# Kernel tuning notes

Hardware: AMD Instinct MI355X
Metric: run time of the kernel (lower is better)

Reference implementation:

```python
import jax, jax.numpy as jnp
import numpy as np

DIM = 512
HID = 1024        # dim * expansion_factor
QK = 128          # query_key_dim
G = 256           # group_size
EPS = 1e-5


def setup_inputs() -> dict:
    key = jax.random.key(0)
    ks = jax.random.split(key, 6)
    x = jax.random.normal(ks[0], (4, 4096, DIM), jnp.float32)
    ln_w = jnp.ones((DIM,), jnp.float32)
    ln_b = jnp.zeros((DIM,), jnp.float32)
    Wh = 0.02 * jax.random.normal(ks[1], (DIM, 2 * HID), jnp.float32)
    bh = jnp.zeros((2 * HID,), jnp.float32)
    Wqk = 0.02 * jax.random.normal(ks[2], (DIM, QK), jnp.float32)
    bqk = jnp.zeros((QK,), jnp.float32)
    gamma = 0.02 * jax.random.normal(ks[3], (4, QK), jnp.float32)  # nn.init.normal_(gamma, std=0.02)
    beta = jnp.zeros((4, QK), jnp.float32)
    Wo = 0.02 * jax.random.normal(ks[4], (HID, DIM), jnp.float32)
    bo = jnp.zeros((DIM,), jnp.float32)
    return {"x": x, "ln_w": ln_w, "ln_b": ln_b, "Wh": Wh, "bh": bh,
            "Wqk": Wqk, "bqk": bqk, "gamma": gamma, "beta": beta,
            "Wo": Wo, "bo": bo}


def reference(x, ln_w, ln_b, Wh, bh, Wqk, bqk, gamma, beta, Wo, bo):
    b, n, _ = x.shape
    g = n // G  # number of groups (n chosen as multiple of G -> no padding)

    # LayerNorm (torch uses biased variance)
    mu = jnp.mean(x, axis=-1, keepdims=True)
    var = jnp.mean((x - mu) ** 2, axis=-1, keepdims=True)
    normed = (x - mu) * jax.lax.rsqrt(var + EPS) * ln_w + ln_b

    # to_hidden: Linear -> SiLU, split into v / gate
    h = jax.nn.silu(normed @ Wh + bh)            # [b, n, 2*HID]
    v, gate = jnp.split(h, 2, axis=-1)           # each [b, n, HID]

    # to_qk: Linear -> SiLU, then 4-head offset/scale
    qk = jax.nn.silu(normed @ Wqk + bqk)         # [b, n, QK]
    qkh = qk[..., None, :] * gamma + beta        # [b, n, 4, QK]
    quad_q, lin_q, quad_k, lin_k = (qkh[..., i, :] for i in range(4))

    # group: b (g n) d -> b g n d
    grp = lambda t: t.reshape(b, g, G, t.shape[-1])
    qq, qk_, lq, lk, vv = map(grp, (quad_q, quad_k, lin_q, lin_k, v))

    # quadratic (group-local) attention with ReLU^2 scores, causal within group
    sim = jnp.einsum('bgid,bgjd->bgij', qq, qk_) / G
    attn = jnp.square(jnp.maximum(sim, 0.0))
    causal_mask = jnp.triu(jnp.ones((G, G), dtype=bool), 1)
    attn = jnp.where(causal_mask, 0.0, attn)
    quad_out = jnp.einsum('bgij,bgje->bgie', attn, vv)   # [b, g, G, HID]

    # linear attention across groups: per-group kv, exclusive cumsum over group dim
    lin_kv = jnp.einsum('bgnd,bgne->bgde', lk, vv) / G   # [b, g, QK, HID]
    lin_kv = jnp.cumsum(lin_kv, axis=1)
    lin_kv = jnp.pad(lin_kv, ((0, 0), (1, 0), (0, 0), (0, 0)))[:, :-1]
    lin_out = jnp.einsum('bgde,bgnd->bgne', lin_kv, lq)  # [b, g, G, HID]

    out = gate * (quad_out.reshape(b, n, HID) + lin_out.reshape(b, n, HID))
    return out @ Wo + bo + x
```

## Files before the change

### kernel.cpp

```cpp
#include <hip/hip_runtime.h>
#include <hip/hip_bf16.h>
#include <math.h>


#define BATCH 4
#define SEQ   4096
#define TROWS 16384
#define DIMD  512
#define HIDD  1024
#define QKD   128
#define GRP   256
#define NGRP  16
#define BGRP  64
#define EPIW  132
#define EPB   130

typedef unsigned short bfraw;
typedef __attribute__((ext_vector_type(8))) short bf16x8;
typedef __attribute__((ext_vector_type(8))) unsigned short u16x8;
typedef __attribute__((ext_vector_type(4))) unsigned int u32x4;
typedef __attribute__((ext_vector_type(4))) float f32x4;

__device__ __forceinline__ float bf2f(bfraw u) {
    union { float f; unsigned int i; } c;
    c.i = ((unsigned int)u) << 16;
    return c.f;
}
__device__ __forceinline__ bfraw f2bf(float f) {
    unsigned int x = __float_as_uint(f);
    unsigned int r = (x + 0x7fffu + ((x >> 16) & 1u)) >> 16;
    return (bfraw)r;
}
__device__ __forceinline__ unsigned int pkbf(float lo, float hi) {
    __hip_bfloat162 h2 = __float22bfloat162_rn(make_float2(lo, hi));
    union { __hip_bfloat162 h; unsigned int u; } c; c.h = h2;
    return c.u;
}
__device__ __forceinline__ void store16bf(bfraw* dst, const float* src) {
    u32x4 a, b;
    #pragma unroll
    for (int k = 0; k < 4; ++k) a[k] = pkbf(src[2 * k], src[2 * k + 1]);
    #pragma unroll
    for (int k = 0; k < 4; ++k) b[k] = pkbf(src[8 + 2 * k], src[8 + 2 * k + 1]);
    *(u32x4*)dst = a;
    *(u32x4*)(dst + 8) = b;
}
__device__ __forceinline__ float silu_f(float z) {
    return z / (1.f + __expf(-z));
}
__device__ __forceinline__ void gload_lds16(const void* g, void* l) {
    __builtin_amdgcn_global_load_lds(
        (const __attribute__((address_space(1))) unsigned int*)g,
        (__attribute__((address_space(3))) unsigned int*)l, 16, 0, 0);
}

__device__ __forceinline__ void mfma_step(const bfraw* As, const bfraw* Bs,
                                          f32x4 acc[4][4], int wm, int wn,
                                          int q, int mi) {
    bf16x8 af[4], bfg[4];
    #pragma unroll
    for (int i = 0; i < 4; ++i)
        af[i] = *(const bf16x8*)&As[(size_t)(wm * 64 + i * 16 + mi) * 32 + q * 8];
    #pragma unroll
    for (int j = 0; j < 4; ++j)
        bfg[j] = *(const bf16x8*)&Bs[(size_t)(wn * 64 + j * 16 + mi) * 32 + q * 8];
    #pragma unroll
    for (int i = 0; i < 4; ++i)
        #pragma unroll
        for (int j = 0; j < 4; ++j)
            acc[i][j] = __builtin_amdgcn_mfma_f32_16x16x32_bf16(af[i], bfg[j], acc[i][j], 0, 0, 0);
}

#define SMEMP_DECL                                              \
    __shared__ __align__(16) char smem_[33280];                 \
    bfraw* A0buf = (bfraw*)smem_;                               \
    bfraw* B0buf = (bfraw*)(smem_ + 8192);                      \
    bfraw* A1buf = (bfraw*)(smem_ + 16384);                     \
    bfraw* B1buf = (bfraw*)(smem_ + 24576);

#define PIPE_DSTS                                               \
    bfraw* a0d  = A0buf + wid * 512;                            \
    bfraw* a0d2 = A0buf + 2048 + wid * 512;                     \
    bfraw* b0d  = B0buf + wid * 512;                            \
    bfraw* b0d2 = B0buf + 2048 + wid * 512;                     \
    bfraw* a1d  = A1buf + wid * 512;                            \
    bfraw* a1d2 = A1buf + 2048 + wid * 512;                     \
    bfraw* b1d  = B1buf + wid * 512;                            \
    bfraw* b1d2 = B1buf + 2048 + wid * 512;

#define KLOOP_PRE(Abase, Astr, Bbase, Bstr)                                    \
    const bfraw* pa0 = (Abase) + (size_t)(t >> 2) * (Astr) + (t & 3) * 8;      \
    const bfraw* pa1 = pa0 + (size_t)64 * (Astr);                              \
    const bfraw* pb0 = (Bbase) + (size_t)(t >> 2) * (Bstr) + (t & 3) * 8;      \
    const bfraw* pb1 = pb0 + (size_t)64 * (Bstr);

#define STAGE0                                                                 \
    do { gload_lds16(pa0, a0d); gload_lds16(pa1, a0d2);                        \
         gload_lds16(pb0, b0d); gload_lds16(pb1, b0d2);                        \
         pa0 += 32; pa1 += 32; pb0 += 32; pb1 += 32; } while (0)
#define STAGE1                                                                 \
    do { gload_lds16(pa0, a1d); gload_lds16(pa1, a1d2);                        \
         gload_lds16(pb0, b1d); gload_lds16(pb1, b1d2);                        \
         pa0 += 32; pa1 += 32; pb0 += 32; pb1 += 32; } while (0)

#define PIPE_LOOP(NIT, Abase, Astr, Bbase, Bstr)                               \
    {                                                                          \
        KLOOP_PRE(Abase, Astr, Bbase, Bstr)                                    \
        STAGE0;                                                                \
        for (int it = 0; it < (NIT); it += 2) {                                \
            __syncthreads();                                                   \
            if (it + 1 < (NIT)) STAGE1;                                        \
            mfma_step(A0buf, B0buf, acc, wm, wn, q, mi);                       \
            __syncthreads();                                                   \
            if (it + 2 < (NIT)) STAGE0;                                        \
            if (it + 1 < (NIT))                                                \
                mfma_step(A1buf, B1buf, acc, wm, wn, q, mi);                   \
        }                                                                      \
        __syncthreads();                                                       \
    }

__device__ __forceinline__ int epi_row(int p, int lr) {
    return (lr < 16) ? (p * 16 + lr) : (64 + p * 16 + (lr - 16));
}

__global__ __launch_bounds__(256) void prep_kernel(const float* __restrict__ x,
                                                   const float* __restrict__ lnw,
                                                   const float* __restrict__ lnb,
                                                   const float* __restrict__ Wh,
                                                   const float* __restrict__ Wo,
                                                   const float* __restrict__ Wqk,
                                                   bfraw* __restrict__ normb,
                                                   bfraw* __restrict__ WhT,
                                                   bfraw* __restrict__ WoT,
                                                   bfraw* __restrict__ WqkT) {
    __shared__ float tile[32][33];
    int bid = blockIdx.x;
    int t = threadIdx.x;
    if (bid < 4096) {
        int row  = bid * 4 + (t >> 6);
        int lane = t & 63;
        const float* xr = x + (size_t)row * DIMD;
        float4 v0 = ((const float4*)xr)[lane];
        float4 v1 = ((const float4*)xr)[lane + 64];
        float s  = v0.x + v0.y + v0.z + v0.w + v1.x + v1.y + v1.z + v1.w;
        float ss = v0.x*v0.x + v0.y*v0.y + v0.z*v0.z + v0.w*v0.w
                 + v1.x*v1.x + v1.y*v1.y + v1.z*v1.z + v1.w*v1.w;
        #pragma unroll
        for (int off = 32; off; off >>= 1) {
            s  += __shfl_xor(s, off);
            ss += __shfl_xor(ss, off);
        }
        float mu  = s * (1.f / DIMD);
        float var = ss * (1.f / DIMD) - mu * mu;
        float inv = rsqrtf(var + 1e-5f);
        float4 w0 = ((const float4*)lnw)[lane],  w1 = ((const float4*)lnw)[lane + 64];
        float4 b0 = ((const float4*)lnb)[lane],  b1 = ((const float4*)lnb)[lane + 64];
        unsigned int o0 = pkbf((v0.x - mu) * inv * w0.x + b0.x,
                               (v0.y - mu) * inv * w0.y + b0.y);
        unsigned int o1 = pkbf((v0.z - mu) * inv * w0.z + b0.z,
                               (v0.w - mu) * inv * w0.w + b0.w);
        unsigned int o2 = pkbf((v1.x - mu) * inv * w1.x + b1.x,
                               (v1.y - mu) * inv * w1.y + b1.y);
        unsigned int o3 = pkbf((v1.z - mu) * inv * w1.z + b1.z,
                               (v1.w - mu) * inv * w1.w + b1.w);
        unsigned int* brow = (unsigned int*)(normb + (size_t)row * DIMD);
        ((uint2*)brow)[lane]      = make_uint2(o0, o1);
        ((uint2*)brow)[lane + 64] = make_uint2(o2, o3);
        return;
    }
    bid -= 4096;
    const float* in; bfraw* outp; int R, C, nx;
    if (bid < 1024)      { in = Wh;  outp = WhT;  R = DIMD; C = 2 * HIDD; nx = 64; }
    else if (bid < 1536) { bid -= 1024; in = Wo;  outp = WoT;  R = HIDD; C = DIMD; nx = 16; }
    else                 { bid -= 1536; in = Wqk; outp = WqkT; R = DIMD; C = QKD;  nx = 4; }
    int c0 = (bid % nx) * 32, r0 = (bid / nx) * 32;
    int tr = t >> 3, tc4 = (t & 7) * 4;
    float4 v = *(const float4*)&in[(size_t)(r0 + tr) * C + c0 + tc4];
    tile[tr][tc4 + 0] = v.x; tile[tr][tc4 + 1] = v.y;
    tile[tr][tc4 + 2] = v.z; tile[tr][tc4 + 3] = v.w;
    __syncthreads();
    ushort4 s;
    s.x = f2bf(tile[tc4 + 0][tr]);
    s.y = f2bf(tile[tc4 + 1][tr]);
    s.z = f2bf(tile[tc4 + 2][tr]);
    s.w = f2bf(tile[tc4 + 3][tr]);
    *(ushort4*)&outp[(size_t)(c0 + tr) * R + r0 + tc4] = s;
}

__global__ __launch_bounds__(512, 2) void gemm_h256(
    const bfraw* __restrict__ A,
    const bfraw* __restrict__ WhT,
    const bfraw* __restrict__ WqkT,
    const float* __restrict__ bh,
    const float* __restrict__ bqk,
    const float* __restrict__ gamma,
    const float* __restrict__ beta,
    bfraw* __restrict__ vT,
    bfraw* __restrict__ gate,
    bfraw* __restrict__ qq,
    bfraw* __restrict__ lq,
    bfraw* __restrict__ kk,
    bfraw* __restrict__ lkT) {
    __shared__ __align__(16) char smem_[131072];
    const int t = threadIdx.x;
    const int lane = t & 63, wid = t >> 6;
    const int wm = wid >> 2, wn = wid & 3;
    const int q = lane >> 4, mi = lane & 15;
    int nid = (blockIdx.x & 7) * 72 + (blockIdx.x >> 3);
    const int ct = nid % 9, by = nid / 9;
    const int r0 = by * 256, c0 = ct * 256;

    const int lslot = (lane & 7) ^ (lane >> 3);
    const int rbase = wid * 16 + (lane >> 3) * 2 + (lslot >> 2);
    const int kel   = (lslot & 3) * 8;
    const bfraw* As0 = A + (size_t)(r0 + rbase) * DIMD + kel;
    const bfraw* As1 = As0 + (size_t)128 * DIMD;
    const bfraw* Bs0; const bfraw* Bs1;
    if (ct < 8) {
        Bs0 = WhT + (size_t)(c0 + rbase) * DIMD + kel;
        Bs1 = Bs0 + (size_t)128 * DIMD;
    } else {
        Bs0 = WqkT + (size_t)rbase * DIMD + kel;
        Bs1 = Bs0;
    }
    const int swz = ((((mi & 1) << 2) | q) ^ ((mi >> 1) & 7)) << 4;
    const int a_off = (wm * 64 + (mi >> 1)) * 128 + swz;
    const int b_off = (wn * 32 + (mi >> 1)) * 128 + swz;
    const int ldst = wid * 1024;

#define GH_STAGE(KT, SLOT)                                                    \
    do {                                                                      \
        char* sb_ = smem_ + (SLOT) * 32768;                                   \
        gload_lds16(As0 + (KT) * 32, sb_ + ldst);                             \
        gload_lds16(As1 + (KT) * 32, sb_ + 8192 + ldst);                      \
        gload_lds16(Bs0 + (KT) * 32, sb_ + 16384 + ldst);                     \
        gload_lds16(Bs1 + (KT) * 32, sb_ + 24576 + ldst);                     \
    } while (0)

    f32x4 acc[8][4] = {};
    GH_STAGE(0, 0);
    GH_STAGE(1, 1);
    GH_STAGE(2, 2);
    asm volatile("s_waitcnt vmcnt(8)" ::: "memory");
    __builtin_amdgcn_s_barrier();

    #pragma unroll
    for (int j = 0; j < 16; ++j) {
        if (j + 3 < 16) GH_STAGE(j + 3, (j + 3) & 3);
        const char* cb = smem_ + (j & 3) * 32768;
        bf16x8 af[8], bfr[4];
        #pragma unroll
        for (int mf = 0; mf < 8; ++mf)
            af[mf] = *(const bf16x8*)(cb + a_off + mf * 1024);
        #pragma unroll
        for (int nf = 0; nf < 4; ++nf)
            bfr[nf] = *(const bf16x8*)(cb + 16384 + b_off + nf * 1024);
        __builtin_amdgcn_s_setprio(1);
        #pragma unroll
        for (int mf = 0; mf < 8; ++mf)
            #pragma unroll
            for (int nf = 0; nf < 4; ++nf)
                acc[mf][nf] = __builtin_amdgcn_mfma_f32_16x16x32_bf16(
                    af[mf], bfr[nf], acc[mf][nf], 0, 0, 0);
        __builtin_amdgcn_s_setprio(0);
        if (j + 3 < 16)      asm volatile("s_waitcnt vmcnt(8)" ::: "memory");
        else if (j + 2 < 16) asm volatile("s_waitcnt vmcnt(4)" ::: "memory");
        else if (j + 1 < 16) asm volatile("s_waitcnt vmcnt(0)" ::: "memory");
        __builtin_amdgcn_s_barrier();
    }
#undef GH_STAGE

    float* epi = (float*)smem_;
    if (ct == 8) {
        float* gbl = (float*)(smem_ + 33792);
        gbl[t] = gamma[t];
        gbl[t + 512] = beta[t];
        float bq4[4];
        #pragma unroll
        for (int nf = 0; nf < 4; ++nf)
            bq4[nf] = (wn < 2) ? bqk[wn * 64 + nf * 16 + mi] : 0.f;
        #pragma unroll
        for (int p = 0; p < 4; ++p) {
            if (wm == (p >> 1) && wn < 2) {
                #pragma unroll
                for (int m2 = 0; m2 < 4; ++m2) {
                    int mf = ((p & 1) << 2) + m2;
                    #pragma unroll
                    for (int nf = 0; nf < 4; ++nf)
                        #pragma unroll
                        for (int rg = 0; rg < 4; ++rg)
                            epi[(m2 * 16 + q * 4 + rg) * 132 + wn * 64 + nf * 16 + mi] =
                                silu_f(acc[mf][nf][rg] + bq4[nf]);
                }
            }
            __syncthreads();
            {
                int lr = t >> 3, cs = (t & 7) * 16;
                float z[16];
                #pragma unroll
                for (int k = 0; k < 16; ++k) z[k] = epi[lr * 132 + cs + k];
                size_t growr = (size_t)(r0 + p * 64 + lr) * QKD + cs;
                #pragma unroll
                for (int hd = 0; hd < 3; ++hd) {
                    bfraw* arr = (hd == 0) ? qq : (hd == 1) ? lq : kk;
                    float tmp[16];
                    #pragma unroll
                    for (int k = 0; k < 16; ++k)
                        tmp[k] = z[k] * gbl[hd * 128 + cs + k] + gbl[512 + hd * 128 + cs + k];
                    store16bf(arr + growr, tmp);
                }
            }
            {
                int c = t >> 2, jh = (t & 3) * 16;
                float g3 = gbl[384 + c], e3 = gbl[896 + c];
                float tmp[16];
                #pragma unroll
                for (int k = 0; k < 16; ++k)
                    tmp[k] = epi[(jh + k) * 132 + c] * g3 + e3;
                store16bf(lkT + ((size_t)by * QKD + c) * GRP + p * 64 + jh, tmp);
            }
            __syncthreads();
        }
        return;
    }
    float bias4[4];
    #pragma unroll
    for (int nf = 0; nf < 4; ++nf)
        bias4[nf] = bh[c0 + wn * 64 + nf * 16 + mi];
    if (ct < 4) {
        #pragma unroll
        for (int p = 0; p < 4; ++p) {
            if (wm == (p >> 1)) {
                #pragma unroll
                for (int m2 = 0; m2 < 4; ++m2) {
                    int mf = ((p & 1) << 2) + m2;
                    #pragma unroll
                    for (int nf = 0; nf < 4; ++nf)
                        #pragma unroll
                        for (int rg = 0; rg < 4; ++rg)
                            epi[(m2 * 16 + q * 4 + rg) * 257 + wn * 64 + nf * 16 + mi] =
                                silu_f(acc[mf][nf][rg] + bias4[nf]);
                }
            }
            __syncthreads();
            int e2 = t >> 1, js = (t & 1) * 32;
            bfraw* dst = vT + ((size_t)by * HIDD + c0 + e2) * GRP + p * 64 + js;
            #pragma unroll
            for (int h2 = 0; h2 < 2; ++h2) {
                float tmp[16];
                #pragma unroll
                for (int k = 0; k < 16; ++k)
                    tmp[k] = epi[(js + h2 * 16 + k) * 257 + e2];
                store16bf(dst + h2 * 16, tmp);
            }
            __syncthreads();
        }
    } else {
        #pragma unroll
        for (int p = 0; p < 4; ++p) {
            if (wm == (p >> 1)) {
                #pragma unroll
                for (int m2 = 0; m2 < 4; ++m2) {
                    int mf = ((p & 1) << 2) + m2;
                    #pragma unroll
                    for (int nf = 0; nf < 4; ++nf)
                        #pragma unroll
                        for (int rg = 0; rg < 4; ++rg)
                            epi[(m2 * 16 + q * 4 + rg) * 260 + wn * 64 + nf * 16 + mi] =
                                silu_f(acc[mf][nf][rg] + bias4[nf]);
                }
            }
            __syncthreads();
            int lr = t >> 3, cs = (t & 7) * 32;
            const float* src = epi + lr * 260 + cs;
            bfraw* dst = gate + (size_t)(r0 + p * 64 + lr) * HIDD + (c0 - HIDD) + cs;
            #pragma unroll
            for (int h2 = 0; h2 < 2; ++h2) {
                float tmp[16];
                #pragma unroll
                for (int k = 0; k < 16; ++k) tmp[k] = src[h2 * 16 + k];
                store16bf(dst + h2 * 16, tmp);
            }
            __syncthreads();
        }
    }
}

__global__ __launch_bounds__(256) void simkv_kernel(const bfraw* __restrict__ qq,
                                                    const bfraw* __restrict__ kk,
                                                    bfraw* __restrict__ attn,
                                                    const bfraw* __restrict__ vT,
                                                    const bfraw* __restrict__ lkT,
                                                    bfraw* __restrict__ kvT_raw) {
    SMEMP_DECL
    float* epi = (float*)smem_;
    int t = threadIdx.x;
    int lane = t & 63, wid = t >> 6;
    int wm = wid >> 1, wn = wid & 1;
    int q = lane >> 4, mi = lane & 15;
    int bid = blockIdx.x;
    f32x4 acc[4][4] = {};
    PIPE_DSTS
    if (bid < 512) {
        int bg = bid >> 3;
        int row0 = (bid & 7) * 128;
        PIPE_LOOP(8, vT + (size_t)bg * HIDD * GRP + (size_t)row0 * GRP, GRP,
                  lkT + (size_t)bg * QKD * GRP, GRP)
        bfraw* outg = kvT_raw + (size_t)bg * HIDD * QKD;
        #pragma unroll
        for (int p = 0; p < 4; ++p) {
            #pragma unroll
            for (int j = 0; j < 4; ++j)
                #pragma unroll
                for (int rg = 0; rg < 4; ++rg)
                    epi[(wm * 16 + q * 4 + rg) * EPIW + wn * 64 + j * 16 + mi] = acc[p][j][rg];
            __syncthreads();
            int lr = t >> 3, c0t = (t & 7) * 16;
            int gr = row0 + epi_row(p, lr);
            store16bf(outg + (size_t)gr * QKD + c0t, &epi[lr * EPIW + c0t]);
            __syncthreads();
        }
        return;
    }
    int i = bid - 512;
    int bg = i & 63;
    int tid = i >> 6;
    int ry = (tid == 0) ? 0 : 1;
    int rx = (tid == 2) ? 1 : 0;
    int row0 = ry * 128, col0 = rx * 128;
    PIPE_LOOP(4, qq + (size_t)(bg * GRP + row0) * QKD, QKD,
              kk + (size_t)(bg * GRP + col0) * QKD, QKD)
    bfraw* ag = attn + (size_t)bg * GRP * GRP;
    #pragma unroll
    for (int p = 0; p < 4; ++p) {
        #pragma unroll
        for (int j = 0; j < 4; ++j) {
            int colg = col0 + wn * 64 + j * 16 + mi;
            #pragma unroll
            for (int rg = 0; rg < 4; ++rg) {
                int rowg = row0 + wm * 64 + p * 16 + q * 4 + rg;
                float s = acc[p][j][rg] * (1.f / GRP);
                s = fmaxf(s, 0.f);
                s = s * s;
                epi[(wm * 16 + q * 4 + rg) * EPIW + wn * 64 + j * 16 + mi] =
                    (colg > rowg) ? 0.f : s;
            }
        }
        __syncthreads();
        int lr = t >> 3, c0t = (t & 7) * 16;
        int gr = row0 + epi_row(p, lr);
        store16bf(ag + (size_t)gr * GRP + col0 + c0t, &epi[lr * EPIW + c0t]);
        __syncthreads();
    }
}

__global__ __launch_bounds__(256) void cumsum2_kernel(const bfraw* __restrict__ raw,
                                                      bfraw* __restrict__ ex) {
    int idx = blockIdx.x * 256 + threadIdx.x;
    int b = idx >> 17;
    int r = idx & 131071;
    const bfraw* rp = raw + (size_t)b * NGRP * 131072 + r;
    bfraw* ep = ex + (size_t)b * NGRP * 131072 + r;
    float run = 0.f;
    #pragma unroll
    for (int g = 0; g < NGRP; ++g) {
        ep[(size_t)g * 131072] = f2bf(run);
        run += bf2f(rp[(size_t)g * 131072]) * (1.f / GRP);
    }
}

__global__ __launch_bounds__(256) void quadlin_mfma(const bfraw* __restrict__ attn,
                                                    const bfraw* __restrict__ vT,
                                                    const bfraw* __restrict__ lq,
                                                    const bfraw* __restrict__ kvT_ex,
                                                    const bfraw* __restrict__ gate,
                                                    bfraw* __restrict__ gated) {
    int bg = blockIdx.z;
    int row0 = blockIdx.y * 128;
    int col0 = blockIdx.x * 128;
    SMEMP_DECL
    float* epi = (float*)smem_;
    int t = threadIdx.x;
    int lane = t & 63, wid = t >> 6;
    int wm = wid >> 1, wn = wid & 1;
    int q = lane >> 4, mi = lane & 15;
    f32x4 acc[4][4] = {};
    PIPE_DSTS
    {
        int nit = (row0 + 128) >> 5;
        PIPE_LOOP(nit, attn + (size_t)bg * GRP * GRP + (size_t)row0 * GRP, GRP,
                  vT + (size_t)bg * HIDD * GRP + (size_t)col0 * GRP, GRP)
    }
    PIPE_LOOP(4, lq + (size_t)(bg * GRP + row0) * QKD, QKD,
              kvT_ex + (size_t)bg * HIDD * QKD + (size_t)col0 * QKD, QKD)
    #pragma unroll
    for (int p = 0; p < 4; ++p) {
        #pragma unroll
        for (int j = 0; j < 4; ++j)
            #pragma unroll
            for (int rg = 0; rg < 4; ++rg)
                epi[(wm * 16 + q * 4 + rg) * EPIW + wn * 64 + j * 16 + mi] = acc[p][j][rg];
        __syncthreads();
        int lr = t >> 3, c0t = (t & 7) * 16;
        int gr = row0 + epi_row(p, lr);
        size_t grow = (size_t)bg * GRP + gr;
        const float* src = &epi[lr * EPIW + c0t];
        const bfraw* gsrc = gate + grow * HIDD + col0 + c0t;
        u16x8 g0 = *(const u16x8*)gsrc;
        u16x8 g1 = *(const u16x8*)(gsrc + 8);
        float tmp[16];
        #pragma unroll
        for (int k = 0; k < 8; ++k) tmp[k] = src[k] * bf2f(g0[k]);
        #pragma unroll
        for (int k = 0; k < 8; ++k) tmp[8 + k] = src[8 + k] * bf2f(g1[k]);
        store16bf(gated + grow * HIDD + col0 + c0t, tmp);
        __syncthreads();
    }
}

__global__ __launch_bounds__(256) void gemm_final(const bfraw* __restrict__ A,
                                                  const bfraw* __restrict__ BT,
                                                  const float* __restrict__ bo,
                                                  const float* __restrict__ x,
                                                  float* __restrict__ out) {
    SMEMP_DECL
    float* epi = (float*)smem_;
    int t = threadIdx.x;
    int lane = t & 63, wid = t >> 6;
    int wm = wid >> 1, wn = wid & 1;
    int q = lane >> 4, mi = lane & 15;
    int row0 = blockIdx.y * 128, col0 = blockIdx.x * 128;
    f32x4 acc[4][4] = {};
    PIPE_DSTS
    PIPE_LOOP(32, A + (size_t)row0 * HIDD, HIDD, BT + (size_t)col0 * HIDD, HIDD)
    #pragma unroll
    for (int p = 0; p < 4; ++p) {
        #pragma unroll
        for (int j = 0; j < 4; ++j) {
            float bv = bo[col0 + wn * 64 + j * 16 + mi];
            #pragma unroll
            for (int rg = 0; rg < 4; ++rg)
                epi[(wm * 16 + q * 4 + rg) * EPIW + wn * 64 + j * 16 + mi] =
                    acc[p][j][rg] + bv;
        }
        __syncthreads();
        int lr = t >> 3, c0t = (t & 7) * 16;
        int gr = row0 + epi_row(p, lr);
        const float* src = &epi[lr * EPIW + c0t];
        const float* xsrc = x + (size_t)gr * DIMD + col0 + c0t;
        float* dst = out + (size_t)gr * DIMD + col0 + c0t;
        #pragma unroll
        for (int v = 0; v < 4; ++v) {
            float4 a = ((const float4*)src)[v];
            float4 xv = ((const float4*)xsrc)[v];
            a.x += xv.x; a.y += xv.y; a.z += xv.z; a.w += xv.w;
            ((float4*)dst)[v] = a;
        }
        __syncthreads();
    }
}

extern "C" void kernel_launch(void* const* d_in, const int* in_sizes, int n_in,
                              void* d_out, int out_size, void* d_ws, size_t ws_size,
                              hipStream_t stream) {
    const float* x     = (const float*)d_in[0];
    const float* ln_w  = (const float*)d_in[1];
    const float* ln_b  = (const float*)d_in[2];
    const float* Wh    = (const float*)d_in[3];
    const float* bh    = (const float*)d_in[4];
    const float* Wqk   = (const float*)d_in[5];
    const float* bqk   = (const float*)d_in[6];
    const float* gamma = (const float*)d_in[7];
    const float* beta  = (const float*)d_in[8];
    const float* Wo    = (const float*)d_in[9];
    const float* bo    = (const float*)d_in[10];
    float* out = (float*)d_out;

    char* outb_ = (char*)d_out;
    bfraw* attn = (bfraw*)(outb_);
    bfraw* qq   = (bfraw*)(outb_ + 8388608);
    bfraw* kk   = (bfraw*)(outb_ + 12582912);
    bfraw* lq   = (bfraw*)(outb_ + 16777216);
    bfraw* WhT  = (bfraw*)(outb_ + 20971520);
    bfraw* WqkT = (bfraw*)(outb_ + 23068672);

    char* wsb = (char*)d_ws;
    bfraw* vT      = (bfraw*)(wsb);
    bfraw* gate    = (bfraw*)(wsb + 33554432);
    bfraw* gated   = (bfraw*)(wsb + 67108864);
    bfraw* normb   = (bfraw*)(wsb + 100663296);
    bfraw* kvT_raw = (bfraw*)(wsb + 117440512);
    bfraw* kvT_ex  = (bfraw*)(wsb + 134217728);
    bfraw* lkT     = (bfraw*)(wsb + 150994944);
    bfraw* WoT     = (bfraw*)(wsb + 155189248);

    prep_kernel<<<4096 + 1024 + 512 + 64, 256, 0, stream>>>(
        x, ln_w, ln_b, Wh, Wo, Wqk, normb, WhT, WoT, WqkT);
    gemm_h256<<<576, 512, 0, stream>>>(
        normb, WhT, WqkT, bh, bqk, gamma, beta, vT, gate, qq, lq, kk, lkT);
    simkv_kernel<<<512 + 192, 256, 0, stream>>>(qq, kk, attn, vT, lkT, kvT_raw);
    cumsum2_kernel<<<(BATCH * QKD * HIDD) / 256, 256, 0, stream>>>(kvT_raw, kvT_ex);
    quadlin_mfma<<<dim3(HIDD / 128, GRP / 128, BGRP), 256, 0, stream>>>(
        attn, vT, lq, kvT_ex, gate, gated);
    gemm_final<<<dim3(DIMD / 128, TROWS / 128), 256, 0, stream>>>(gated, WoT, bo, x, out);
}
```

Baseline: 278.5 us.

## Split GEMM k-step into two halves interleaving LDS reads, prefetch and MFMA

Splits each k-iteration of the hidden-projection GEMM into two phases. Each phase loads half the A fragments from LDS, issues half of the next global-to-LDS prefetch (A then B), and runs its half of the MFMAs, in a ping-pong style schedule. The aim is to overlap LDS reads and global loads with matrix work and to reduce register pressure from holding all eight A fragments. It adds extra workgroup barriers per iteration, which may cost more than the overlap gains.

```diff
diff --git a/kernel.cpp b/kernel.cpp
--- a/kernel.cpp
+++ b/kernel.cpp
@@ -236,6 +236,18 @@
         gload_lds16(Bs0 + (KT) * 32, sb_ + 16384 + ldst);                     \
         gload_lds16(Bs1 + (KT) * 32, sb_ + 24576 + ldst);                     \
     } while (0)
+#define GH_STAGE_A(KT, SLOT)                                                  \
+    do {                                                                      \
+        char* sb_ = smem_ + (SLOT) * 32768;                                   \
+        gload_lds16(As0 + (KT) * 32, sb_ + ldst);                             \
+        gload_lds16(As1 + (KT) * 32, sb_ + 8192 + ldst);                      \
+    } while (0)
+#define GH_STAGE_B(KT, SLOT)                                                  \
+    do {                                                                      \
+        char* sb_ = smem_ + (SLOT) * 32768;                                   \
+        gload_lds16(Bs0 + (KT) * 32, sb_ + 16384 + ldst);                     \
+        gload_lds16(Bs1 + (KT) * 32, sb_ + 24576 + ldst);                     \
+    } while (0)
 
     f32x4 acc[8][4] = {};
     GH_STAGE(0, 0);
@@ -246,29 +258,48 @@
 
     #pragma unroll
     for (int j = 0; j < 16; ++j) {
-        if (j + 3 < 16) GH_STAGE(j + 3, (j + 3) & 3);
         const char* cb = smem_ + (j & 3) * 32768;
-        bf16x8 af[8], bfr[4];
-        #pragma unroll
-        for (int mf = 0; mf < 8; ++mf)
-            af[mf] = *(const bf16x8*)(cb + a_off + mf * 1024);
+        bf16x8 af0[4], af1[4], bfr[4];
+        #pragma unroll
+        for (int mf = 0; mf < 4; ++mf)
+            af0[mf] = *(const bf16x8*)(cb + a_off + mf * 1024);
         #pragma unroll
         for (int nf = 0; nf < 4; ++nf)
             bfr[nf] = *(const bf16x8*)(cb + 16384 + b_off + nf * 1024);
+        if (j + 3 < 16) GH_STAGE_A(j + 3, (j + 3) & 3);
+        __builtin_amdgcn_s_barrier();
+        asm volatile("s_waitcnt lgkmcnt(0)");
         __builtin_amdgcn_s_setprio(1);
         #pragma unroll
-        for (int mf = 0; mf < 8; ++mf)
+        for (int mf = 0; mf < 4; ++mf)
             #pragma unroll
             for (int nf = 0; nf < 4; ++nf)
                 acc[mf][nf] = __builtin_amdgcn_mfma_f32_16x16x32_bf16(
-                    af[mf], bfr[nf], acc[mf][nf], 0, 0, 0);
+                    af0[mf], bfr[nf], acc[mf][nf], 0, 0, 0);
         __builtin_amdgcn_s_setprio(0);
+        __builtin_amdgcn_s_barrier();
+        #pragma unroll
+        for (int mf = 0; mf < 4; ++mf)
+            af1[mf] = *(const bf16x8*)(cb + a_off + (4 + mf) * 1024);
+        if (j + 3 < 16) GH_STAGE_B(j + 3, (j + 3) & 3);
         if (j + 3 < 16)      asm volatile("s_waitcnt vmcnt(8)" ::: "memory");
         else if (j + 2 < 16) asm volatile("s_waitcnt vmcnt(4)" ::: "memory");
         else if (j + 1 < 16) asm volatile("s_waitcnt vmcnt(0)" ::: "memory");
         __builtin_amdgcn_s_barrier();
+        asm volatile("s_waitcnt lgkmcnt(0)");
+        __builtin_amdgcn_s_setprio(1);
+        #pragma unroll
+        for (int mf = 0; mf < 4; ++mf)
+            #pragma unroll
+            for (int nf = 0; nf < 4; ++nf)
+                acc[4 + mf][nf] = __builtin_amdgcn_mfma_f32_16x16x32_bf16(
+                    af1[mf], bfr[nf], acc[4 + mf][nf], 0, 0, 0);
+        __builtin_amdgcn_s_setprio(0);
+        __builtin_amdgcn_s_barrier();
     }
 #undef GH_STAGE
+#undef GH_STAGE_A
+#undef GH_STAGE_B
 
     float* epi = (float*)smem_;
     if (ct == 8) {
```

New measurement: 340.8 us. 22.4% more time.

## Split hidden GEMM across 16 waves per block with smaller per-wave tiles

Applied to the files above, without the earlier changes.

The fused hidden/qk GEMM block grows from 512 to 1024 threads. Each wave now computes a 64x64 sub-tile instead of 128x64, which halves its accumulator registers, and each thread issues one A and one B async load per stage. The next-stage global prefetch is moved after the LDS fragment reads, and the epilogue remapping is adjusted to the new thread count. The aim is more waves in flight to hide latency, at the cost of less fragment reuse per wave, more LDS reads per MFMA and a tighter register budget.

```diff
diff --git a/kernel.cpp b/kernel.cpp
--- a/kernel.cpp
+++ b/kernel.cpp
@@ -187,7 +187,7 @@
     *(ushort4*)&outp[(size_t)(c0 + tr) * R + r0 + tc4] = s;
 }
 
-__global__ __launch_bounds__(512, 2) void gemm_h256(
+__global__ __launch_bounds__(1024, 4) void gemm_h256(
     const bfraw* __restrict__ A,
     const bfraw* __restrict__ WhT,
     const bfraw* __restrict__ WqkT,
@@ -210,61 +210,55 @@
     const int ct = nid % 9, by = nid / 9;
     const int r0 = by * 256, c0 = ct * 256;
 
-    const int lslot = (lane & 7) ^ (lane >> 3);
-    const int rbase = wid * 16 + (lane >> 3) * 2 + (lslot >> 2);
-    const int kel   = (lslot & 3) * 8;
-    const bfraw* As0 = A + (size_t)(r0 + rbase) * DIMD + kel;
-    const bfraw* As1 = As0 + (size_t)128 * DIMD;
-    const bfraw* Bs0; const bfraw* Bs1;
+    const int lslot = (t & 7) ^ ((t >> 3) & 7);
+    const int srow  = 2 * (t >> 3) + (lslot >> 2);
+    const int skel  = (lslot & 3) * 8;
+    const bfraw* Asrc = A + (size_t)(r0 + srow) * DIMD + skel;
+    const bfraw* Bsrc;
     if (ct < 8) {
-        Bs0 = WhT + (size_t)(c0 + rbase) * DIMD + kel;
-        Bs1 = Bs0 + (size_t)128 * DIMD;
+        Bsrc = WhT + (size_t)(c0 + srow) * DIMD + skel;
     } else {
-        Bs0 = WqkT + (size_t)rbase * DIMD + kel;
-        Bs1 = Bs0;
+        Bsrc = WqkT + (size_t)(srow & 127) * DIMD + skel;
     }
     const int swz = ((((mi & 1) << 2) | q) ^ ((mi >> 1) & 7)) << 4;
-    const int a_off = (wm * 64 + (mi >> 1)) * 128 + swz;
+    const int a_off = (wm * 32 + (mi >> 1)) * 128 + swz;
     const int b_off = (wn * 32 + (mi >> 1)) * 128 + swz;
-    const int ldst = wid * 1024;
 
 #define GH_STAGE(KT, SLOT)                                                    \
     do {                                                                      \
         char* sb_ = smem_ + (SLOT) * 32768;                                   \
-        gload_lds16(As0 + (KT) * 32, sb_ + ldst);                             \
-        gload_lds16(As1 + (KT) * 32, sb_ + 8192 + ldst);                      \
-        gload_lds16(Bs0 + (KT) * 32, sb_ + 16384 + ldst);                     \
-        gload_lds16(Bs1 + (KT) * 32, sb_ + 24576 + ldst);                     \
+        gload_lds16(Asrc + (KT) * 32, sb_ + t * 16);                          \
+        gload_lds16(Bsrc + (KT) * 32, sb_ + 16384 + t * 16);                  \
     } while (0)
 
-    f32x4 acc[8][4] = {};
+    f32x4 acc[4][4] = {};
     GH_STAGE(0, 0);
     GH_STAGE(1, 1);
     GH_STAGE(2, 2);
-    asm volatile("s_waitcnt vmcnt(8)" ::: "memory");
+    asm volatile("s_waitcnt vmcnt(4)" ::: "memory");
     __builtin_amdgcn_s_barrier();
 
     #pragma unroll
     for (int j = 0; j < 16; ++j) {
-        if (j + 3 < 16) GH_STAGE(j + 3, (j + 3) & 3);
         const char* cb = smem_ + (j & 3) * 32768;
-        bf16x8 af[8], bfr[4];
-        #pragma unroll
-        for (int mf = 0; mf < 8; ++mf)
+        bf16x8 af[4], bfr[4];
+        #pragma unroll
+        for (int mf = 0; mf < 4; ++mf)
             af[mf] = *(const bf16x8*)(cb + a_off + mf * 1024);
         #pragma unroll
         for (int nf = 0; nf < 4; ++nf)
             bfr[nf] = *(const bf16x8*)(cb + 16384 + b_off + nf * 1024);
+        if (j + 3 < 16) GH_STAGE(j + 3, (j + 3) & 3);
         __builtin_amdgcn_s_setprio(1);
         #pragma unroll
-        for (int mf = 0; mf < 8; ++mf)
+        for (int mf = 0; mf < 4; ++mf)
             #pragma unroll
             for (int nf = 0; nf < 4; ++nf)
                 acc[mf][nf] = __builtin_amdgcn_mfma_f32_16x16x32_bf16(
                     af[mf], bfr[nf], acc[mf][nf], 0, 0, 0);
         __builtin_amdgcn_s_setprio(0);
-        if (j + 3 < 16)      asm volatile("s_waitcnt vmcnt(8)" ::: "memory");
-        else if (j + 2 < 16) asm volatile("s_waitcnt vmcnt(4)" ::: "memory");
+        if (j + 3 < 16)      asm volatile("s_waitcnt vmcnt(4)" ::: "memory");
+        else if (j + 2 < 16) asm volatile("s_waitcnt vmcnt(2)" ::: "memory");
         else if (j + 1 < 16) asm volatile("s_waitcnt vmcnt(0)" ::: "memory");
         __builtin_amdgcn_s_barrier();
     }
@@ -272,29 +266,26 @@
 
     float* epi = (float*)smem_;
     if (ct == 8) {
-        float* gbl = (float*)(smem_ + 33792);
-        gbl[t] = gamma[t];
-        gbl[t + 512] = beta[t];
+        float* gbl = (float*)(smem_ + 67584);
+        if (t < 512) { gbl[t] = gamma[t]; gbl[t + 512] = beta[t]; }
         float bq4[4];
         #pragma unroll
         for (int nf = 0; nf < 4; ++nf)
             bq4[nf] = (wn < 2) ? bqk[wn * 64 + nf * 16 + mi] : 0.f;
         #pragma unroll
         for (int p = 0; p < 4; ++p) {
-            if (wm == (p >> 1) && wn < 2) {
-                #pragma unroll
-                for (int m2 = 0; m2 < 4; ++m2) {
-                    int mf = ((p & 1) << 2) + m2;
+            if (wm == p && wn < 2) {
+                #pragma unroll
+                for (int mf = 0; mf < 4; ++mf)
                     #pragma unroll
                     for (int nf = 0; nf < 4; ++nf)
                         #pragma unroll
                         for (int rg = 0; rg < 4; ++rg)
-                            epi[(m2 * 16 + q * 4 + rg) * 132 + wn * 64 + nf * 16 + mi] =
+                            epi[(mf * 16 + q * 4 + rg) * 132 + wn * 64 + nf * 16 + mi] =
                                 silu_f(acc[mf][nf][rg] + bq4[nf]);
-                }
             }
             __syncthreads();
-            {
+            if (t < 512) {
                 int lr = t >> 3, cs = (t & 7) * 16;
                 float z[16];
                 #pragma unroll
@@ -309,9 +300,9 @@
                         tmp[k] = z[k] * gbl[hd * 128 + cs + k] + gbl[512 + hd * 128 + cs + k];
                     store16bf(arr + growr, tmp);
                 }
-            }
-            {
-                int c = t >> 2, jh = (t & 3) * 16;
+            } else {
+                int tt = t - 512;
+                int c = tt >> 2, jh = (tt & 3) * 16;
                 float g3 = gbl[384 + c], e3 = gbl[896 + c];
                 float tmp[16];
                 #pragma unroll
@@ -330,57 +321,45 @@
     if (ct < 4) {
         #pragma unroll
         for (int p = 0; p < 4; ++p) {
-            if (wm == (p >> 1)) {
-                #pragma unroll
-                for (int m2 = 0; m2 < 4; ++m2) {
-                    int mf = ((p & 1) << 2) + m2;
+            if (wm == p) {
+                #pragma unroll
+                for (int mf = 0; mf < 4; ++mf)
                     #pragma unroll
                     for (int nf = 0; nf < 4; ++nf)
                         #pragma unroll
                         for (int rg = 0; rg < 4; ++rg)
-                            epi[(m2 * 16 + q * 4 + rg) * 257 + wn * 64 + nf * 16 + mi] =
+                            epi[(mf * 16 + q * 4 + rg) * 257 + wn * 64 + nf * 16 + mi] =
                                 silu_f(acc[mf][nf][rg] + bias4[nf]);
-                }
             }
             __syncthreads();
-            int e2 = t >> 1, js = (t & 1) * 32;
-            bfraw* dst = vT + ((size_t)by * HIDD + c0 + e2) * GRP + p * 64 + js;
-            #pragma unroll
-            for (int h2 = 0; h2 < 2; ++h2) {
-                float tmp[16];
-                #pragma unroll
-                for (int k = 0; k < 16; ++k)
-                    tmp[k] = epi[(js + h2 * 16 + k) * 257 + e2];
-                store16bf(dst + h2 * 16, tmp);
-            }
+            int e2 = t >> 2, js = (t & 3) * 16;
+            float tmp[16];
+            #pragma unroll
+            for (int k = 0; k < 16; ++k)
+                tmp[k] = epi[(js + k) * 257 + e2];
+            store16bf(vT + ((size_t)by * HIDD + c0 + e2) * GRP + p * 64 + js, tmp);
             __syncthreads();
         }
     } else {
         #pragma unroll
         for (int p = 0; p < 4; ++p) {
-            if (wm == (p >> 1)) {
-                #pragma unroll
-                for (int m2 = 0; m2 < 4; ++m2) {
-                    int mf = ((p & 1) << 2) + m2;
+            if (wm == p) {
+                #pragma unroll
+                for (int mf = 0; mf < 4; ++mf)
                     #pragma unroll
                     for (int nf = 0; nf < 4; ++nf)
                         #pragma unroll
                         for (int rg = 0; rg < 4; ++rg)
-                            epi[(m2 * 16 + q * 4 + rg) * 260 + wn * 64 + nf * 16 + mi] =
+                            epi[(mf * 16 + q * 4 + rg) * 260 + wn * 64 + nf * 16 + mi] =
                                 silu_f(acc[mf][nf][rg] + bias4[nf]);
-                }
             }
             __syncthreads();
-            int lr = t >> 3, cs = (t & 7) * 32;
-            const float* src = epi + lr * 260 + cs;
-            bfraw* dst = gate + (size_t)(r0 + p * 64 + lr) * HIDD + (c0 - HIDD) + cs;
-            #pragma unroll
-            for (int h2 = 0; h2 < 2; ++h2) {
-                float tmp[16];
-                #pragma unroll
-                for (int k = 0; k < 16; ++k) tmp[k] = src[h2 * 16 + k];
-                store16bf(dst + h2 * 16, tmp);
-            }
+            int lr = t >> 4, cs = (t & 15) * 16;
+            float tmp[16];
+            #pragma unroll
+            for (int k = 0; k < 16; ++k)
+                tmp[k] = epi[lr * 260 + cs + k];
+            store16bf(gate + (size_t)(r0 + p * 64 + lr) * HIDD + (c0 - HIDD) + cs, tmp);
             __syncthreads();
         }
     }
@@ -596,7 +575,7 @@
 
     prep_kernel<<<4096 + 1024 + 512 + 64, 256, 0, stream>>>(
         x, ln_w, ln_b, Wh, Wo, Wqk, normb, WhT, WoT, WqkT);
-    gemm_h256<<<576, 512, 0, stream>>>(
+    gemm_h256<<<576, 1024, 0, stream>>>(
         normb, WhT, WqkT, bh, bqk, gamma, beta, vT, gate, qq, lq, kk, lkT);
     simkv_kernel<<<512 + 192, 256, 0, stream>>>(qq, kk, attn, vT, lkT, kvT_raw);
     cumsum2_kernel<<<(BATCH * QKD * HIDD) / 256, 256, 0, stream>>>(kvT_raw, kvT_ex);
```

New measurement: 272.9 us. -2.0%, faster.
